# Kernel optimization log

Hardware: AMD Instinct MI355X
Metric: run time of the kernel (lower is better)

## Reference

```python
import jax, jax.numpy as jnp
import numpy as np

N, R, M = 2048, 8, 4096  # samples, rank, signal length (M even)


def setup_inputs() -> dict:
    key = jax.random.key(0)
    kW, kH, kT = jax.random.split(key, 3)
    W = jax.random.normal(kW, (N, R), dtype=jnp.float32)
    H = jax.random.normal(kH, (R, M), dtype=jnp.float32)
    # tau are per-(sample, component) time shifts; modest positive values
    tau = jax.random.uniform(kT, (N, R), dtype=jnp.float32) * 5.0
    return {"W": W, "H": H, "tau": tau}


def reference(W, H, tau):
    # W: (N, R) raw weights, H: (R, M) raw sources, tau: (N, R) shifts
    M_ = H.shape[1]
    Nf = M_ // 2 + 1
    # one-sided spectrum of the (softplus-constrained) sources
    Hf = jnp.fft.fft(jax.nn.softplus(H), axis=1)[:, :Nf]            # (R, Nf) complex
    # rebuild full mirrored spectrum: [Hf, conj(flip(Hf[:, 1:Nf-1]))] -> (R, M)
    Hft = jnp.concatenate([Hf, jnp.conj(Hf[:, 1:Nf - 1][:, ::-1])], axis=1)
    f = jnp.arange(M_, dtype=H.dtype) / M_                          # (M,) normalized freqs
    # complex exponential shift operator, (N, R, M)
    omega = jnp.exp(-2j * jnp.pi * jnp.einsum('nd,m->ndm', tau, f))
    Wf = jax.nn.softplus(W)[:, :, None] * omega                     # (N, R, M)
    # reduce over rank: V[n, m] = sum_d Wf[n, d, m] * Hft[d, m]
    V = jnp.einsum('ndm,dm->nm', Wf, Hft)                           # (N, M) complex
    return V
```

## Files before the change

kernel.cpp:

```cpp
#include <hip/hip_runtime.h>
#include <math.h>

#define MLEN 4096
#define LOG2M 12
#define RANK 8
#define NSAMP 2048
#define VEC 8
#define NS  4

__device__ __forceinline__ float softplus_f(float x) {
    return (x > 20.0f) ? x : log1pf(expf(x));
}

__global__ __launch_bounds__(1024) void fft_rows_kernel(const float* __restrict__ H,
                                                        float2* __restrict__ Hft) {
    __shared__ float2 buf[MLEN];
    const int d = blockIdx.x;
    const float* row = H + d * MLEN;

    for (int i = threadIdx.x; i < MLEN; i += 1024) {
        int src = (int)(__brev((unsigned)i) >> (32 - LOG2M));
        buf[i] = make_float2(softplus_f(row[src]), 0.0f);
    }
    __syncthreads();

    for (int s = 1; s <= LOG2M; ++s) {
        const int half = 1 << (s - 1);
#pragma unroll 2
        for (int p = threadIdx.x; p < (MLEN >> 1); p += 1024) {
            const int k  = p & (half - 1);
            const int i0 = ((p >> (s - 1)) << s) + k;
            const int i1 = i0 + half;
            const float ang = -6.28318530717958647692f * (float)k / (float)(half << 1);
            const float sw = __sinf(ang);
            const float cw = __cosf(ang);
            float2 a = buf[i0];
            float2 b = buf[i1];
            float tr = b.x * cw - b.y * sw;
            float ti = b.x * sw + b.y * cw;
            buf[i0] = make_float2(a.x + tr, a.y + ti);
            buf[i1] = make_float2(a.x - tr, a.y - ti);
        }
        __syncthreads();
    }

    float2* outrow = Hft + d * MLEN;
    for (int i = threadIdx.x; i < MLEN; i += 1024) outrow[i] = buf[i];
}

template <int REAL_ONLY>
__global__ __launch_bounds__(256) void mix_kernel(const float* __restrict__ W,
                                                  const float* __restrict__ tau,
                                                  const float2* __restrict__ Hft,
                                                  float* __restrict__ out) {
    const int tid = threadIdx.x;
    const int m0  = blockIdx.x * (256 * VEC) + tid;
    const int n0  = blockIdx.y * NS;

    __shared__ float s_spw[NS * RANK];
    __shared__ float s_tau[NS * RANK];
    if (tid < NS * RANK) {
        s_spw[tid] = softplus_f(W[n0 * RANK + tid]);
        s_tau[tid] = tau[n0 * RANK + tid];
    }
    __syncthreads();

    float ar[NS][VEC];
    float ai[NS][VEC];
#pragma unroll
    for (int j = 0; j < NS; ++j)
#pragma unroll
        for (int k = 0; k < VEC; ++k) { ar[j][k] = 0.0f; ai[j][k] = 0.0f; }

    const float th0f = -6.28318530717958647692f * ((float)m0 * (1.0f / (float)MLEN));
    const float dthf = -6.28318530717958647692f * (256.0f / (float)MLEN);

#pragma unroll
    for (int d = 0; d < RANK; ++d) {
        float cs[NS], sn[NS], dc[NS], ds[NS];
#pragma unroll
        for (int j = 0; j < NS; ++j) {
            const float t   = s_tau[j * RANK + d];
            const float spw = s_spw[j * RANK + d];
            const float a0 = th0f * t;
            const float a1 = dthf * t;
            const float c0 = __cosf(a0);
            const float s0 = __sinf(a0);
            dc[j] = __cosf(a1);
            ds[j] = __sinf(a1);
            cs[j] = spw * c0;
            sn[j] = spw * s0;
        }
        const float2* __restrict__ hrow = Hft + d * MLEN + m0;
        float2 hv[VEC];
#pragma unroll
        for (int k = 0; k < VEC; ++k) hv[k] = hrow[k * 256];
#pragma unroll
        for (int k = 0; k < VEC; ++k) {
#pragma unroll
            for (int j = 0; j < NS; ++j) {
                ar[j][k] += cs[j] * hv[k].x - sn[j] * hv[k].y;
                if (!REAL_ONLY) ai[j][k] += cs[j] * hv[k].y + sn[j] * hv[k].x;
                const float ncs = cs[j] * dc[j] - sn[j] * ds[j];
                sn[j] = cs[j] * ds[j] + sn[j] * dc[j];
                cs[j] = ncs;
            }
        }
    }

#pragma unroll
    for (int j = 0; j < NS; ++j) {
#pragma unroll
        for (int k = 0; k < VEC; ++k) {
            const size_t idx = (size_t)(n0 + j) * MLEN + m0 + k * 256;
            if (REAL_ONLY) out[idx] = ar[j][k];
            else ((float2*)out)[idx] = make_float2(ar[j][k], ai[j][k]);
        }
    }
}

extern "C" void kernel_launch(void* const* d_in, const int* in_sizes, int n_in,
                              void* d_out, int out_size, void* d_ws, size_t ws_size,
                              hipStream_t stream) {
    const float* W   = (const float*)d_in[0];
    const float* H   = (const float*)d_in[1];
    const float* tau = (const float*)d_in[2];
    float2* Hft = (float2*)d_ws;
    float* out  = (float*)d_out;

    fft_rows_kernel<<<RANK, 1024, 0, stream>>>(H, Hft);

    const long long NM = (long long)NSAMP * MLEN;
    dim3 grid(MLEN / (256 * VEC), NSAMP / NS);
    if ((long long)out_size >= 2 * NM) {
        mix_kernel<0><<<grid, 256, 0, stream>>>(W, tau, Hft, out);
    } else {
        mix_kernel<1><<<grid, 256, 0, stream>>>(W, tau, Hft, out);
    }
}
```

Baseline: 33.15 us.

## Switch row FFT to radix-4 and precompute phase-step twiddles in mix kernel

The per-row FFT changes from twelve radix-2 stages to six radix-4 stages, with base-4 digit-reversed input ordering, which halves the number of barriers and shared-memory passes. The mix kernel now computes each (sample, rank) phase-step cos/sin once per block into shared memory instead of once per thread. It also skips the unused final rotation update, stops unrolling the rank loop, and sets a minimum of four blocks per CU in launch bounds to limit register use. The FFT is small next to the mix kernel, so most of the effect depends on the mix changes, and the tighter occupancy bound could force register spills.

```diff
diff --git a/kernel.cpp b/kernel.cpp
--- a/kernel.cpp
+++ b/kernel.cpp
@@ -2,7 +2,6 @@
 #include <math.h>
 
 #define MLEN 4096
-#define LOG2M 12
 #define RANK 8
 #define NSAMP 2048
 #define VEC 8
@@ -19,28 +18,43 @@
     const float* row = H + d * MLEN;
 
     for (int i = threadIdx.x; i < MLEN; i += 1024) {
-        int src = (int)(__brev((unsigned)i) >> (32 - LOG2M));
+        unsigned x = __brev((unsigned)i) >> 20;
+        unsigned src = ((x & 0x555u) << 1) | ((x & 0xAAAu) >> 1);
         buf[i] = make_float2(softplus_f(row[src]), 0.0f);
     }
     __syncthreads();
 
-    for (int s = 1; s <= LOG2M; ++s) {
-        const int half = 1 << (s - 1);
-#pragma unroll 2
-        for (int p = threadIdx.x; p < (MLEN >> 1); p += 1024) {
-            const int k  = p & (half - 1);
-            const int i0 = ((p >> (s - 1)) << s) + k;
-            const int i1 = i0 + half;
-            const float ang = -6.28318530717958647692f * (float)k / (float)(half << 1);
-            const float sw = __sinf(ang);
-            const float cw = __cosf(ang);
-            float2 a = buf[i0];
-            float2 b = buf[i1];
-            float tr = b.x * cw - b.y * sw;
-            float ti = b.x * sw + b.y * cw;
-            buf[i0] = make_float2(a.x + tr, a.y + ti);
-            buf[i1] = make_float2(a.x - tr, a.y - ti);
-        }
+    for (int s = 0; s < 6; ++s) {
+        const int quarter = 1 << (2 * s);
+        const int p  = threadIdx.x;
+        const int k  = p & (quarter - 1);
+        const int j  = p >> (2 * s);
+        const int i0 = (j << (2 * s + 2)) + k;
+        const int i1 = i0 + quarter;
+        const int i2 = i1 + quarter;
+        const int i3 = i2 + quarter;
+        const float ang = -6.28318530717958647692f * (float)k / (float)(quarter << 2);
+        const float c1 = __cosf(ang), s1 = __sinf(ang);
+        const float c2 = c1 * c1 - s1 * s1, s2 = 2.0f * c1 * s1;
+        const float c3 = c1 * c2 - s1 * s2, s3 = c1 * s2 + s1 * c2;
+
+        float2 a = buf[i0];
+        float2 b = buf[i1];
+        float2 c = buf[i2];
+        float2 e = buf[i3];
+        b = make_float2(b.x * c1 - b.y * s1, b.x * s1 + b.y * c1);
+        c = make_float2(c.x * c2 - c.y * s2, c.x * s2 + c.y * c2);
+        e = make_float2(e.x * c3 - e.y * s3, e.x * s3 + e.y * c3);
+
+        const float2 t0 = make_float2(a.x + c.x, a.y + c.y);
+        const float2 t1 = make_float2(a.x - c.x, a.y - c.y);
+        const float2 t2 = make_float2(b.x + e.x, b.y + e.y);
+        const float2 t3 = make_float2(b.y - e.y, e.x - b.x);
+
+        buf[i0] = make_float2(t0.x + t2.x, t0.y + t2.y);
+        buf[i1] = make_float2(t1.x + t3.x, t1.y + t3.y);
+        buf[i2] = make_float2(t0.x - t2.x, t0.y - t2.y);
+        buf[i3] = make_float2(t1.x - t3.x, t1.y - t3.y);
         __syncthreads();
     }
 
@@ -49,19 +63,23 @@
 }
 
 template <int REAL_ONLY>
-__global__ __launch_bounds__(256) void mix_kernel(const float* __restrict__ W,
-                                                  const float* __restrict__ tau,
-                                                  const float2* __restrict__ Hft,
-                                                  float* __restrict__ out) {
+__global__ __launch_bounds__(256, 4) void mix_kernel(const float* __restrict__ W,
+                                                     const float* __restrict__ tau,
+                                                     const float2* __restrict__ Hft,
+                                                     float* __restrict__ out) {
     const int tid = threadIdx.x;
     const int m0  = blockIdx.x * (256 * VEC) + tid;
     const int n0  = blockIdx.y * NS;
 
-    __shared__ float s_spw[NS * RANK];
-    __shared__ float s_tau[NS * RANK];
+    __shared__ float  s_spw[NS * RANK];
+    __shared__ float  s_tau[NS * RANK];
+    __shared__ float2 s_step[NS * RANK];
     if (tid < NS * RANK) {
+        const float t = tau[n0 * RANK + tid];
         s_spw[tid] = softplus_f(W[n0 * RANK + tid]);
-        s_tau[tid] = tau[n0 * RANK + tid];
+        s_tau[tid] = t;
+        const float a1 = -0.39269908169872415481f * t;
+        s_step[tid] = make_float2(__cosf(a1), __sinf(a1));
     }
     __syncthreads();
 
@@ -73,23 +91,20 @@
         for (int k = 0; k < VEC; ++k) { ar[j][k] = 0.0f; ai[j][k] = 0.0f; }
 
     const float th0f = -6.28318530717958647692f * ((float)m0 * (1.0f / (float)MLEN));
-    const float dthf = -6.28318530717958647692f * (256.0f / (float)MLEN);
 
-#pragma unroll
+#pragma unroll 1
     for (int d = 0; d < RANK; ++d) {
         float cs[NS], sn[NS], dc[NS], ds[NS];
 #pragma unroll
         for (int j = 0; j < NS; ++j) {
             const float t   = s_tau[j * RANK + d];
             const float spw = s_spw[j * RANK + d];
-            const float a0 = th0f * t;
-            const float a1 = dthf * t;
-            const float c0 = __cosf(a0);
-            const float s0 = __sinf(a0);
-            dc[j] = __cosf(a1);
-            ds[j] = __sinf(a1);
-            cs[j] = spw * c0;
-            sn[j] = spw * s0;
+            const float a0  = th0f * t;
+            cs[j] = spw * __cosf(a0);
+            sn[j] = spw * __sinf(a0);
+            const float2 st = s_step[j * RANK + d];
+            dc[j] = st.x;
+            ds[j] = st.y;
         }
         const float2* __restrict__ hrow = Hft + d * MLEN + m0;
         float2 hv[VEC];
@@ -101,9 +116,11 @@
             for (int j = 0; j < NS; ++j) {
                 ar[j][k] += cs[j] * hv[k].x - sn[j] * hv[k].y;
                 if (!REAL_ONLY) ai[j][k] += cs[j] * hv[k].y + sn[j] * hv[k].x;
-                const float ncs = cs[j] * dc[j] - sn[j] * ds[j];
-                sn[j] = cs[j] * ds[j] + sn[j] * dc[j];
-                cs[j] = ncs;
+                if (k < VEC - 1) {
+                    const float ncs = cs[j] * dc[j] - sn[j] * ds[j];
+                    sn[j] = cs[j] * ds[j] + sn[j] * dc[j];
+                    cs[j] = ncs;
+                }
             }
         }
     }
```

Measured after the change: 38.85 us. 1.17x slower.

## Give each thread contiguous frequencies with vectorized loads and stores, one sample per block

Applied to the files above, without the earlier changes.

The mix kernel now assigns each thread 8 contiguous frequency bins, so Hft reads and output writes become 16-byte vector accesses. The twiddle step is a unit frequency increment precomputed per rank in shared memory, and each block handles a single sample instead of four. This drops the reuse of loaded Hft values across 4 samples, so Hft traffic through cache rises fourfold and there are 4x more blocks. Per-thread register pressure falls.

```diff
diff --git a/kernel.cpp b/kernel.cpp
--- a/kernel.cpp
+++ b/kernel.cpp
@@ -6,7 +6,6 @@
 #define RANK 8
 #define NSAMP 2048
 #define VEC 8
-#define NS  4
 
 __device__ __forceinline__ float softplus_f(float x) {
     return (x > 20.0f) ? x : log1pf(expf(x));
@@ -54,67 +53,66 @@
                                                   const float2* __restrict__ Hft,
                                                   float* __restrict__ out) {
     const int tid = threadIdx.x;
-    const int m0  = blockIdx.x * (256 * VEC) + tid;
-    const int n0  = blockIdx.y * NS;
+    const int m0  = (blockIdx.x * 256 + tid) * VEC;
+    const int n   = blockIdx.y;
 
-    __shared__ float s_spw[NS * RANK];
-    __shared__ float s_tau[NS * RANK];
-    if (tid < NS * RANK) {
-        s_spw[tid] = softplus_f(W[n0 * RANK + tid]);
-        s_tau[tid] = tau[n0 * RANK + tid];
+    __shared__ float  s_spw[RANK];
+    __shared__ float  s_tau[RANK];
+    __shared__ float2 s_step[RANK];
+    if (tid < RANK) {
+        const float t = tau[n * RANK + tid];
+        s_spw[tid] = softplus_f(W[n * RANK + tid]);
+        s_tau[tid] = t;
+        const float a1 = -1.53398078788564122971e-3f * t;
+        s_step[tid] = make_float2(__cosf(a1), __sinf(a1));
     }
     __syncthreads();
 
-    float ar[NS][VEC];
-    float ai[NS][VEC];
+    float ar[VEC];
+    float ai[VEC];
 #pragma unroll
-    for (int j = 0; j < NS; ++j)
-#pragma unroll
-        for (int k = 0; k < VEC; ++k) { ar[j][k] = 0.0f; ai[j][k] = 0.0f; }
+    for (int k = 0; k < VEC; ++k) { ar[k] = 0.0f; ai[k] = 0.0f; }
 
-    const float th0f = -6.28318530717958647692f * ((float)m0 * (1.0f / (float)MLEN));
-    const float dthf = -6.28318530717958647692f * (256.0f / (float)MLEN);
+    const float thm = -6.28318530717958647692f * ((float)m0 * (1.0f / (float)MLEN));
+
+#pragma unroll 1
+    for (int d = 0; d < RANK; ++d) {
+        const float4* hp = reinterpret_cast<const float4*>(Hft + (size_t)d * MLEN + m0);
+        const float4 h0 = hp[0], h1 = hp[1], h2 = hp[2], h3 = hp[3];
+
+        const float t   = s_tau[d];
+        const float a0  = thm * t;
+        const float spw = s_spw[d];
+        float cs = spw * __cosf(a0);
+        float sn = spw * __sinf(a0);
+        const float2 st = s_step[d];
+        const float dc = st.x, ds = st.y;
 
 #pragma unroll
-    for (int d = 0; d < RANK; ++d) {
-        float cs[NS], sn[NS], dc[NS], ds[NS];
-#pragma unroll
-        for (int j = 0; j < NS; ++j) {
-            const float t   = s_tau[j * RANK + d];
-            const float spw = s_spw[j * RANK + d];
-            const float a0 = th0f * t;
-            const float a1 = dthf * t;
-            const float c0 = __cosf(a0);
-            const float s0 = __sinf(a0);
-            dc[j] = __cosf(a1);
-            ds[j] = __sinf(a1);
-            cs[j] = spw * c0;
-            sn[j] = spw * s0;
-        }
-        const float2* __restrict__ hrow = Hft + d * MLEN + m0;
-        float2 hv[VEC];
-#pragma unroll
-        for (int k = 0; k < VEC; ++k) hv[k] = hrow[k * 256];
-#pragma unroll
         for (int k = 0; k < VEC; ++k) {
-#pragma unroll
-            for (int j = 0; j < NS; ++j) {
-                ar[j][k] += cs[j] * hv[k].x - sn[j] * hv[k].y;
-                if (!REAL_ONLY) ai[j][k] += cs[j] * hv[k].y + sn[j] * hv[k].x;
-                const float ncs = cs[j] * dc[j] - sn[j] * ds[j];
-                sn[j] = cs[j] * ds[j] + sn[j] * dc[j];
-                cs[j] = ncs;
+            const float4& hq = (k < 2) ? h0 : (k < 4) ? h1 : (k < 6) ? h2 : h3;
+            const float hx = (k & 1) ? hq.z : hq.x;
+            const float hy = (k & 1) ? hq.w : hq.y;
+            ar[k] += cs * hx - sn * hy;
+            if (!REAL_ONLY) ai[k] += cs * hy + sn * hx;
+            if (k < VEC - 1) {
+                const float ncs = cs * dc - sn * ds;
+                sn = cs * ds + sn * dc;
+                cs = ncs;
             }
         }
     }
 
+    if (REAL_ONLY) {
+        float* po = out + (size_t)n * MLEN + m0;
+        reinterpret_cast<float4*>(po)[0] = make_float4(ar[0], ar[1], ar[2], ar[3]);
+        reinterpret_cast<float4*>(po)[1] = make_float4(ar[4], ar[5], ar[6], ar[7]);
+    } else {
+        float2* po = (float2*)out + (size_t)n * MLEN + m0;
 #pragma unroll
-    for (int j = 0; j < NS; ++j) {
-#pragma unroll
-        for (int k = 0; k < VEC; ++k) {
-            const size_t idx = (size_t)(n0 + j) * MLEN + m0 + k * 256;
-            if (REAL_ONLY) out[idx] = ar[j][k];
-            else ((float2*)out)[idx] = make_float2(ar[j][k], ai[j][k]);
+        for (int q = 0; q < 4; ++q) {
+            reinterpret_cast<float4*>(po)[q] =
+                make_float4(ar[2 * q], ai[2 * q], ar[2 * q + 1], ai[2 * q + 1]);
         }
     }
 }
@@ -131,7 +129,7 @@
     fft_rows_kernel<<<RANK, 1024, 0, stream>>>(H, Hft);
 
     const long long NM = (long long)NSAMP * MLEN;
-    dim3 grid(MLEN / (256 * VEC), NSAMP / NS);
+    dim3 grid(MLEN / (256 * VEC), NSAMP);
     if ((long long)out_size >= 2 * NM) {
         mix_kernel<0><<<grid, 256, 0, stream>>>(W, tau, Hft, out);
     } else {
```

After: 49.84 us. +50.4%, slower.
